# Kernel tuning notes

Measured on AMD Instinct MI355X. Metric: run time of the kernel, lower is better.

## Reference

```python
import jax, jax.numpy as jnp
import numpy as np

N_NODES = 50000
N_EDGES = 800000
IN_FEATS = 1024
LAYERS = [128, 128]
EPS = 1e-5  # BatchNorm1d eps


def setup_inputs() -> dict:
    key = jax.random.key(0)
    ks = jax.random.split(key, 24)
    inp = {}
    inp["in_feat"] = jax.random.normal(ks[0], (N_NODES, IN_FEATS), jnp.float32)
    inp["src"] = jax.random.randint(ks[1], (N_EDGES,), 0, N_NODES, dtype=jnp.int32)
    inp["dst"] = jax.random.randint(ks[2], (N_EDGES,), 0, N_NODES, dtype=jnp.int32)
    dims = [IN_FEATS] + LAYERS
    i = 3
    for l in range(len(LAYERS)):
        din, dout = dims[l], dims[l + 1]
        s = 1.0 / np.sqrt(din)
        inp[f"W{l}"] = jax.random.uniform(ks[i], (din, dout), jnp.float32, -s, s); i += 1
        inp[f"b{l}"] = jnp.zeros((dout,), jnp.float32)
        inp[f"Wr{l}"] = jax.random.uniform(ks[i], (din, dout), jnp.float32, -s, s); i += 1
        inp[f"br{l}"] = jnp.zeros((dout,), jnp.float32)
        inp[f"gamma{l}"] = jnp.ones((dout,), jnp.float32)
        inp[f"beta{l}"] = jnp.zeros((dout,), jnp.float32)
        inp[f"mean{l}"] = jnp.zeros((dout,), jnp.float32)
        inp[f"var{l}"] = jnp.ones((dout,), jnp.float32)
    s = 1.0 / np.sqrt(LAYERS[-1])
    inp["Wd"] = jax.random.uniform(ks[i], (LAYERS[-1], 2), jnp.float32, -s, s)
    inp["bd"] = jnp.zeros((2,), jnp.float32)
    return inp


def gcn_layer(h, src, dst, W, b, Wr, br, gamma, beta, mean, var):
    # dgllife GCNLayer: GraphConv(norm='none', activation=relu) -> residual -> dropout(id, eval) -> BN(eval)
    msg = (h @ W)[src]                                        # [E, dout] gather of transformed src feats
    agg = jax.ops.segment_sum(msg, dst, num_segments=N_NODES)  # scatter-add to dst nodes
    new = jax.nn.relu(agg + b)                                 # GraphConv bias + activation
    res = jax.nn.relu(h @ Wr + br)                             # residual Linear + activation
    new = new + res
    return (new - mean) * jax.lax.rsqrt(var + EPS) * gamma + beta  # BatchNorm1d eval


def reference(in_feat, src, dst,
              W0, b0, Wr0, br0, gamma0, beta0, mean0, var0,
              W1, b1, Wr1, br1, gamma1, beta1, mean1, var1,
              Wd, bd):
    h = gcn_layer(in_feat, src, dst, W0, b0, Wr0, br0, gamma0, beta0, mean0, var0)
    h = gcn_layer(h, src, dst, W1, b1, Wr1, br1, gamma1, beta1, mean1, var1)
    logits = h @ Wd + bd                                       # [N, 2]
    return jax.nn.softmax(logits, axis=1)
```

## Files before the change

kernel.cpp:

```cpp
#include <hip/hip_runtime.h>
#include <math.h>

#define NNODES 50000
#define NEDGES 800000
#define KIN 1024
#define DH 128

typedef __bf16 bf16x8 __attribute__((ext_vector_type(8)));
typedef float floatx4 __attribute__((ext_vector_type(4)));

__global__ void k_zero2(int* __restrict__ a, int* __restrict__ b, int n) {
  int i = blockIdx.x * blockDim.x + threadIdx.x;
  if (i < n) { a[i] = 0; b[i] = 0; }
}

__global__ void k_hist(const int* __restrict__ dst, int* __restrict__ cnt, int E) {
  int i = blockIdx.x * blockDim.x + threadIdx.x;
  if (i < E) atomicAdd(&cnt[dst[i]], 1);
}

__global__ __launch_bounds__(1024) void k_scan_local(const int* __restrict__ cnt,
                                                     int* __restrict__ row_ptr,
                                                     int* __restrict__ bsum, int n) {
  __shared__ int sd[1024];
  int t = threadIdx.x;
  int i = blockIdx.x * 1024 + t;
  int v = (i < n) ? cnt[i] : 0;
  sd[t] = v;
  __syncthreads();
  for (int off = 1; off < 1024; off <<= 1) {
    int tv = (t >= off) ? sd[t - off] : 0;
    __syncthreads();
    sd[t] += tv;
    __syncthreads();
  }
  if (i < n) row_ptr[i] = sd[t] - v;
  if (t == 1023) bsum[blockIdx.x] = sd[t];
}

__global__ void k_scan_sums(const int* __restrict__ bsum, int* __restrict__ boff,
                            int nb, int* __restrict__ row_ptr, int n) {
  int lane = threadIdx.x;
  int v = (lane < nb) ? bsum[lane] : 0;
  int incl = v;
  for (int off = 1; off < 64; off <<= 1) {
    int t = __shfl_up(incl, off);
    if (lane >= off) incl += t;
  }
  boff[lane] = incl - v;
  if (lane == 63) row_ptr[n] = incl;
}

__global__ void k_scan_add(int* __restrict__ row_ptr, const int* __restrict__ boff, int n) {
  int i = blockIdx.x * blockDim.x + threadIdx.x;
  if (i < n) row_ptr[i] += boff[i >> 10];
}

__global__ void k_fill(const int* __restrict__ src, const int* __restrict__ dst,
                       const int* __restrict__ row_ptr, int* __restrict__ cursor,
                       int* __restrict__ csr_src, int E) {
  int i = blockIdx.x * blockDim.x + threadIdx.x;
  if (i < E) {
    int d = dst[i];
    int pos = row_ptr[d] + atomicAdd(&cursor[d], 1);
    csr_src[pos] = src[i];
  }
}

__global__ __launch_bounds__(256) void k_prepB(const float* __restrict__ W,
                                               const float* __restrict__ Wr,
                                               __bf16* __restrict__ Bt, int K, int kbits) {
  int id = blockIdx.x * 256 + threadIdx.x;
  int k = id & (K - 1);
  int n = id >> kbits;
  float v = (n < DH) ? W[(size_t)k * DH + n] : Wr[(size_t)k * DH + (n - DH)];
  Bt[(size_t)n * K + k] = (__bf16)v;
}

__device__ __forceinline__ void load_lds16(const void* g, void* l) {
  __builtin_amdgcn_global_load_lds(
      (const __attribute__((address_space(1))) unsigned int*)g,
      (__attribute__((address_space(3))) unsigned int*)l, 16, 0, 0);
}

#define WAITV(N) asm volatile("s_waitcnt vmcnt(" #N ")" ::: "memory")

template <typename AT, int K>
__global__ __launch_bounds__(512, 2) void k_gemm_mfma(
    const AT* __restrict__ X, const __bf16* __restrict__ Bt,
    const float* __restrict__ br, __bf16* __restrict__ XW,
    float* __restrict__ RES, int M) {
  constexpr int ROWB = (sizeof(AT) == 4) ? 256 : 128;
  constexpr int ABUF = 64 * ROWB;
  constexpr int BBUF = 256 * 64 * 2;
  constexpr int TBUF = ABUF + BBUF;
  __shared__ alignas(16) char smem[3 * TBUF];
  const int tid = threadIdx.x;
  const int lane = tid & 63;
  const int w = tid >> 6;
  const int wr = w >> 2;
  const int wc = w & 3;
  const int l15 = lane & 15;
  const int quad = lane >> 4;
  const int bm0 = blockIdx.x * 64;

  auto stageA = [&](char* abase, int k0) {
    if constexpr (sizeof(AT) == 4) {
#pragma unroll
      for (int i = 0; i < 2; ++i) {
        const int r = w * 8 + i * 4 + (lane >> 4);
        int gr = bm0 + r; if (gr > M - 1) gr = M - 1;
        const int c = (lane & 15) ^ (r & 7);
        load_lds16((const char*)X + ((size_t)gr * K + k0 + c * 4) * 4,
                   abase + (w * 8 + i * 4) * 256);
      }
    } else {
      const int r = w * 8 + (lane >> 3);
      int gr = bm0 + r; if (gr > M - 1) gr = M - 1;
      const int c = (lane & 7) ^ (r & 7);
      load_lds16((const char*)X + ((size_t)gr * K + k0 + c * 8) * 2,
                 abase + w * 8 * 128);
    }
  };
  auto stageB = [&](char* bbase, int k0) {
#pragma unroll
    for (int ii = 0; ii < 4; ++ii) {
      const int wi = ii * 8 + w;
      const int n = wi * 8 + (lane >> 3);
      const int c = lane & 7;
      const int cs = c ^ (n & 7);
      load_lds16((const char*)Bt + (size_t)n * (K * 2) + (size_t)k0 * 2 + cs * 16,
                 bbase + wi * 1024);
    }
  };
  auto stage = [&](int s) {
    char* base = smem + (s % 3) * TBUF;
    stageA(base, s * 64);
    stageB(base + ABUF, s * 64);
  };

  auto readA = [&](const char* abase, int mt, int ks) -> bf16x8 {
    const int r = wr * 32 + mt * 16 + l15;
    const char* rowp = abase + r * ROWB;
    if constexpr (sizeof(AT) == 4) {
      const int x = r & 7;
      const int c0 = ks * 8 + quad * 2;
      const floatx4 u = *(const floatx4*)(rowp + ((c0 ^ x) << 4));
      const floatx4 v = *(const floatx4*)(rowp + (((c0 + 1) ^ x) << 4));
      bf16x8 h;
      h[0] = (__bf16)u[0]; h[1] = (__bf16)u[1]; h[2] = (__bf16)u[2]; h[3] = (__bf16)u[3];
      h[4] = (__bf16)v[0]; h[5] = (__bf16)v[1]; h[6] = (__bf16)v[2]; h[7] = (__bf16)v[3];
      return h;
    } else {
      const int cc = ks * 4 + quad;
      return *(const bf16x8*)(rowp + ((cc ^ (r & 7)) << 4));
    }
  };
  auto readB = [&](const char* bbase, int nt, int ks) -> bf16x8 {
    const int n = wc * 64 + nt * 16 + l15;
    const int ch = (ks * 4 + quad) ^ (n & 7);
    return *(const bf16x8*)(bbase + n * 128 + ch * 16);
  };

  floatx4 acc[2][4];
#pragma unroll
  for (int i = 0; i < 2; ++i)
#pragma unroll
    for (int j = 0; j < 4; ++j) acc[i][j] = (floatx4)0.f;

  constexpr int NS = K / 64;
  stage(0);
  stage(1);

  for (int s = 0; s < NS; ++s) {
    if (s == NS - 1) {
      WAITV(0);
    } else if constexpr (sizeof(AT) == 4) {
      WAITV(6);
    } else {
      WAITV(5);
    }
    __builtin_amdgcn_s_barrier();
    __builtin_amdgcn_sched_barrier(0);
    if (s + 2 < NS) stage(s + 2);
    const char* abase = smem + (s % 3) * TBUF;
    const char* bbase = abase + ABUF;
    bf16x8 af[2][2], bfr[4][2];
#pragma unroll
    for (int mt = 0; mt < 2; ++mt)
#pragma unroll
      for (int ks = 0; ks < 2; ++ks) af[mt][ks] = readA(abase, mt, ks);
#pragma unroll
    for (int nt = 0; nt < 4; ++nt)
#pragma unroll
      for (int ks = 0; ks < 2; ++ks) bfr[nt][ks] = readB(bbase, nt, ks);
#pragma unroll
    for (int ks = 0; ks < 2; ++ks)
#pragma unroll
      for (int mt = 0; mt < 2; ++mt)
#pragma unroll
        for (int nt = 0; nt < 4; ++nt)
          acc[mt][nt] = __builtin_amdgcn_mfma_f32_16x16x32_bf16(af[mt][ks], bfr[nt][ks],
                                                                acc[mt][nt], 0, 0, 0);
  }
  __syncthreads();

  float* Cb = (float*)smem;
#pragma unroll
  for (int half = 0; half < 2; ++half) {
    if (wr == half) {
#pragma unroll
      for (int mt = 0; mt < 2; ++mt)
#pragma unroll
        for (int nt = 0; nt < 4; ++nt)
#pragma unroll
          for (int r = 0; r < 4; ++r)
            Cb[(mt * 16 + quad * 4 + r) * 256 + wc * 64 + nt * 16 + l15] = acc[mt][nt][r];
    }
    __syncthreads();
    const int row = tid >> 4;
    const int seg = tid & 15;
    const int grow = bm0 + half * 32 + row;
    if (grow < M) {
      if (seg < 8) {
        const int c0 = seg * 16;
#pragma unroll
        for (int j = 0; j < 2; ++j) {
          const float4 v0 = *(const float4*)&Cb[row * 256 + c0 + j * 8];
          const float4 v1 = *(const float4*)&Cb[row * 256 + c0 + j * 8 + 4];
          bf16x8 h;
          h[0] = (__bf16)v0.x; h[1] = (__bf16)v0.y; h[2] = (__bf16)v0.z; h[3] = (__bf16)v0.w;
          h[4] = (__bf16)v1.x; h[5] = (__bf16)v1.y; h[6] = (__bf16)v1.z; h[7] = (__bf16)v1.w;
          *(bf16x8*)&XW[(size_t)grow * DH + c0 + j * 8] = h;
        }
      } else {
        const int c0 = (seg - 8) * 16;
#pragma unroll
        for (int j = 0; j < 4; ++j) {
          const float4 v = *(const float4*)&Cb[row * 256 + 128 + c0 + j * 4];
          const float4 bb = *(const float4*)&br[c0 + j * 4];
          *(float4*)&RES[(size_t)grow * DH + c0 + j * 4] =
              make_float4(fmaxf(v.x + bb.x, 0.f), fmaxf(v.y + bb.y, 0.f),
                          fmaxf(v.z + bb.z, 0.f), fmaxf(v.w + bb.w, 0.f));
        }
      }
    }
    __syncthreads();
  }
}

template <int MODE>
__global__ __launch_bounds__(256) void k_agg2(
    const __bf16* __restrict__ XW, const float* __restrict__ RES,
    const int* __restrict__ row_ptr, const int* __restrict__ csr_src,
    const float* __restrict__ b, const float* __restrict__ gamma,
    const float* __restrict__ beta, const float* __restrict__ mean,
    const float* __restrict__ var, const float* __restrict__ Wd,
    const float* __restrict__ bd, void* __restrict__ hout, int M) {
  const int node = (blockIdx.x << 2) + (threadIdx.x >> 6);
  const int lane = threadIdx.x & 63;
  if (node >= M) return;
  const int s = row_ptr[node], e = row_ptr[node + 1];
  const unsigned* xw = (const unsigned*)XW;
  float ax = 0.f, ay = 0.f;
  int i = s;
  for (; i + 3 < e; i += 4) {
    const int s0 = csr_src[i], s1 = csr_src[i + 1], s2 = csr_src[i + 2], s3 = csr_src[i + 3];
    const unsigned u0 = xw[(size_t)s0 * 64 + lane];
    const unsigned u1 = xw[(size_t)s1 * 64 + lane];
    const unsigned u2 = xw[(size_t)s2 * 64 + lane];
    const unsigned u3 = xw[(size_t)s3 * 64 + lane];
    ax += __uint_as_float(u0 << 16) + __uint_as_float(u1 << 16) +
          __uint_as_float(u2 << 16) + __uint_as_float(u3 << 16);
    ay += __uint_as_float(u0 & 0xffff0000u) + __uint_as_float(u1 & 0xffff0000u) +
          __uint_as_float(u2 & 0xffff0000u) + __uint_as_float(u3 & 0xffff0000u);
  }
  for (; i < e; ++i) {
    const unsigned u = xw[(size_t)csr_src[i] * 64 + lane];
    ax += __uint_as_float(u << 16);
    ay += __uint_as_float(u & 0xffff0000u);
  }
  const int f0 = lane << 1;
  const float2 bb = *(const float2*)&b[f0];
  const float2 rr = *(const float2*)&RES[(size_t)node * DH + f0];
  const float2 mm = *(const float2*)&mean[f0];
  const float2 vv = *(const float2*)&var[f0];
  const float2 gg = *(const float2*)&gamma[f0];
  const float2 be = *(const float2*)&beta[f0];
  const float x0 = fmaxf(ax + bb.x, 0.f) + rr.x;
  const float x1 = fmaxf(ay + bb.y, 0.f) + rr.y;
  const float y0 = (x0 - mm.x) * rsqrtf(vv.x + 1e-5f) * gg.x + be.x;
  const float y1 = (x1 - mm.y) * rsqrtf(vv.y + 1e-5f) * gg.y + be.y;
  if (MODE == 0) {
    union { __bf16 h[2]; unsigned u; } pk;
    pk.h[0] = (__bf16)y0;
    pk.h[1] = (__bf16)y1;
    ((unsigned*)hout)[(size_t)node * 64 + lane] = pk.u;
  } else {
    const float4 wv = *(const float4*)&Wd[f0 * 2];
    float l0 = y0 * wv.x + y1 * wv.z;
    float l1 = y0 * wv.y + y1 * wv.w;
#pragma unroll
    for (int off = 32; off > 0; off >>= 1) {
      l0 += __shfl_down(l0, off);
      l1 += __shfl_down(l1, off);
    }
    if (lane == 0) {
      l0 += bd[0];
      l1 += bd[1];
      const float m = fmaxf(l0, l1);
      const float e0 = expf(l0 - m), e1 = expf(l1 - m);
      const float inv = 1.f / (e0 + e1);
      float* out = (float*)hout;
      out[(size_t)node * 2] = e0 * inv;
      out[(size_t)node * 2 + 1] = e1 * inv;
    }
  }
}

extern "C" void kernel_launch(void* const* d_in, const int* in_sizes, int n_in,
                              void* d_out, int out_size, void* d_ws, size_t ws_size,
                              hipStream_t stream) {
  const float* in_feat = (const float*)d_in[0];
  const int* src = (const int*)d_in[1];
  const int* dst = (const int*)d_in[2];
  const float* W0 = (const float*)d_in[3];
  const float* b0 = (const float*)d_in[4];
  const float* Wr0 = (const float*)d_in[5];
  const float* br0 = (const float*)d_in[6];
  const float* gamma0 = (const float*)d_in[7];
  const float* beta0 = (const float*)d_in[8];
  const float* mean0 = (const float*)d_in[9];
  const float* var0 = (const float*)d_in[10];
  const float* W1 = (const float*)d_in[11];
  const float* b1 = (const float*)d_in[12];
  const float* Wr1 = (const float*)d_in[13];
  const float* br1 = (const float*)d_in[14];
  const float* gamma1 = (const float*)d_in[15];
  const float* beta1 = (const float*)d_in[16];
  const float* mean1 = (const float*)d_in[17];
  const float* var1 = (const float*)d_in[18];
  const float* Wd = (const float*)d_in[19];
  const float* bd = (const float*)d_in[20];
  float* out = (float*)d_out;

  char* ws = (char*)d_ws;
  size_t off = 0;
  auto alloc = [&](size_t bytes) {
    void* p = ws + off;
    off += (bytes + 255) & ~(size_t)255;
    return p;
  };
  __bf16* XWb = (__bf16*)alloc(sizeof(__bf16) * (size_t)NNODES * DH);
  __bf16* h1 = (__bf16*)alloc(sizeof(__bf16) * (size_t)NNODES * DH);
  float* RES = (float*)alloc(sizeof(float) * (size_t)NNODES * DH);
  int* cnt = (int*)alloc(sizeof(int) * NNODES);
  int* cursor = (int*)alloc(sizeof(int) * NNODES);
  int* row_ptr = (int*)alloc(sizeof(int) * (NNODES + 1));
  int* csr_src = (int*)alloc(sizeof(int) * NEDGES);
  int* bsum = (int*)alloc(sizeof(int) * 64);
  int* boff = (int*)alloc(sizeof(int) * 64);
  __bf16* Bt0 = (__bf16*)alloc(sizeof(__bf16) * 256 * KIN);
  __bf16* Bt1 = (__bf16*)alloc(sizeof(__bf16) * 256 * DH);

  const int nb = (NNODES + 1023) / 1024;
  k_zero2<<<(NNODES + 255) / 256, 256, 0, stream>>>(cnt, cursor, NNODES);
  k_hist<<<(NEDGES + 255) / 256, 256, 0, stream>>>(dst, cnt, NEDGES);
  k_scan_local<<<nb, 1024, 0, stream>>>(cnt, row_ptr, bsum, NNODES);
  k_scan_sums<<<1, 64, 0, stream>>>(bsum, boff, nb, row_ptr, NNODES);
  k_scan_add<<<(NNODES + 255) / 256, 256, 0, stream>>>(row_ptr, boff, NNODES);
  k_fill<<<(NEDGES + 255) / 256, 256, 0, stream>>>(src, dst, row_ptr, cursor, csr_src, NEDGES);

  k_prepB<<<KIN, 256, 0, stream>>>(W0, Wr0, Bt0, KIN, 10);
  k_prepB<<<DH, 256, 0, stream>>>(W1, Wr1, Bt1, DH, 7);

  const int ggrid = (NNODES + 63) / 64;
  const int agrid = (NNODES + 3) / 4;
  k_gemm_mfma<float, KIN><<<ggrid, 512, 0, stream>>>(in_feat, Bt0, br0, XWb, RES, NNODES);
  k_agg2<0><<<agrid, 256, 0, stream>>>(XWb, RES, row_ptr, csr_src, b0, gamma0, beta0,
                                       mean0, var0, nullptr, nullptr, h1, NNODES);
  k_gemm_mfma<__bf16, DH><<<ggrid, 512, 0, stream>>>(h1, Bt1, br1, XWb, RES, NNODES);
  k_agg2<1><<<agrid, 256, 0, stream>>>(XWb, RES, row_ptr, csr_src, b1, gamma1, beta1,
                                       mean1, var1, Wd, bd, out, NNODES);
}
```

Before: 551.5 us.

## Halve fp32 GEMM K-tile to cut LDS and raise occupancy; add nontemporal A loads

For the fp32-input GEMM (the first layer, K=1024), the K step drops from 64 to 32, shrinking the LDS per stage so four 512-thread blocks can fit per CU instead of two (launch bounds raised). The A-operand loads into LDS now use a nontemporal cache hint, since X is streamed once. MFMA sections are wrapped in s_setprio to favour issuing the compute. The cost is twice as many pipeline stages and barriers for the fp32 path, and the higher occupancy target may force register pressure or spills.

```diff
diff --git a/kernel.cpp b/kernel.cpp
--- a/kernel.cpp
+++ b/kernel.cpp
@@ -82,17 +82,24 @@
       (const __attribute__((address_space(1))) unsigned int*)g,
       (__attribute__((address_space(3))) unsigned int*)l, 16, 0, 0);
 }
+__device__ __forceinline__ void load_lds16_nt(const void* g, void* l) {
+  __builtin_amdgcn_global_load_lds(
+      (const __attribute__((address_space(1))) unsigned int*)g,
+      (__attribute__((address_space(3))) unsigned int*)l, 16, 0, 2 );
+}
 
 #define WAITV(N) asm volatile("s_waitcnt vmcnt(" #N ")" ::: "memory")
 
 template <typename AT, int K>
-__global__ __launch_bounds__(512, 2) void k_gemm_mfma(
+__global__ __launch_bounds__(512, 4) void k_gemm_mfma(
     const AT* __restrict__ X, const __bf16* __restrict__ Bt,
     const float* __restrict__ br, __bf16* __restrict__ XW,
     float* __restrict__ RES, int M) {
-  constexpr int ROWB = (sizeof(AT) == 4) ? 256 : 128;
+  constexpr int BK = (sizeof(AT) == 4) ? 32 : 64;
+  constexpr int ROWB = 128;
   constexpr int ABUF = 64 * ROWB;
-  constexpr int BBUF = 256 * 64 * 2;
+  constexpr int BROWB = BK * 2;
+  constexpr int BBUF = 256 * BROWB;
   constexpr int TBUF = ABUF + BBUF;
   __shared__ alignas(16) char smem[3 * TBUF];
   const int tid = threadIdx.x;
@@ -104,47 +111,48 @@
   const int quad = lane >> 4;
   const int bm0 = blockIdx.x * 64;
 
-  auto stageA = [&](char* abase, int k0) {
-    if constexpr (sizeof(AT) == 4) {
-#pragma unroll
-      for (int i = 0; i < 2; ++i) {
-        const int r = w * 8 + i * 4 + (lane >> 4);
-        int gr = bm0 + r; if (gr > M - 1) gr = M - 1;
-        const int c = (lane & 15) ^ (r & 7);
-        load_lds16((const char*)X + ((size_t)gr * K + k0 + c * 4) * 4,
-                   abase + (w * 8 + i * 4) * 256);
+  auto stage = [&](int s2) {
+    char* base = smem + (s2 % 3) * TBUF;
+    {
+      const int r = w * 8 + (lane >> 3);
+      int gr = bm0 + r; if (gr > M - 1) gr = M - 1;
+      const int cs = (lane & 7) ^ (r & 7);
+      if constexpr (sizeof(AT) == 4) {
+        load_lds16_nt((const char*)X + ((size_t)gr * K + s2 * BK + cs * 4) * 4,
+                      base + w * 1024);
+      } else {
+        load_lds16_nt((const char*)X + ((size_t)gr * K + s2 * BK + cs * 8) * 2,
+                      base + w * 1024);
+      }
+    }
+    char* bbase = base + ABUF;
+    if constexpr (BK == 32) {
+#pragma unroll
+      for (int ii = 0; ii < 2; ++ii) {
+        const int wi = ii * 8 + w;
+        const int n = wi * 16 + (lane >> 2);
+        const int cs = (lane & 3) ^ (n & 3);
+        load_lds16((const char*)Bt + (size_t)n * (K * 2) + (size_t)(s2 * BK) * 2 + cs * 16,
+                   bbase + wi * 1024);
       }
     } else {
-      const int r = w * 8 + (lane >> 3);
-      int gr = bm0 + r; if (gr > M - 1) gr = M - 1;
-      const int c = (lane & 7) ^ (r & 7);
-      load_lds16((const char*)X + ((size_t)gr * K + k0 + c * 8) * 2,
-                 abase + w * 8 * 128);
-    }
-  };
-  auto stageB = [&](char* bbase, int k0) {
-#pragma unroll
-    for (int ii = 0; ii < 4; ++ii) {
-      const int wi = ii * 8 + w;
-      const int n = wi * 8 + (lane >> 3);
-      const int c = lane & 7;
-      const int cs = c ^ (n & 7);
-      load_lds16((const char*)Bt + (size_t)n * (K * 2) + (size_t)k0 * 2 + cs * 16,
-                 bbase + wi * 1024);
-    }
-  };
-  auto stage = [&](int s) {
-    char* base = smem + (s % 3) * TBUF;
-    stageA(base, s * 64);
-    stageB(base + ABUF, s * 64);
+#pragma unroll
+      for (int ii = 0; ii < 4; ++ii) {
+        const int wi = ii * 8 + w;
+        const int n = wi * 8 + (lane >> 3);
+        const int cs = (lane & 7) ^ (n & 7);
+        load_lds16((const char*)Bt + (size_t)n * (K * 2) + (size_t)(s2 * BK) * 2 + cs * 16,
+                   bbase + wi * 1024);
+      }
+    }
   };
 
   auto readA = [&](const char* abase, int mt, int ks) -> bf16x8 {
     const int r = wr * 32 + mt * 16 + l15;
     const char* rowp = abase + r * ROWB;
+    const int x = r & 7;
     if constexpr (sizeof(AT) == 4) {
-      const int x = r & 7;
-      const int c0 = ks * 8 + quad * 2;
+      const int c0 = quad * 2;
       const floatx4 u = *(const floatx4*)(rowp + ((c0 ^ x) << 4));
       const floatx4 v = *(const floatx4*)(rowp + (((c0 + 1) ^ x) << 4));
       bf16x8 h;
@@ -153,13 +161,18 @@
       return h;
     } else {
       const int cc = ks * 4 + quad;
-      return *(const bf16x8*)(rowp + ((cc ^ (r & 7)) << 4));
+      return *(const bf16x8*)(rowp + ((cc ^ x) << 4));
     }
   };
   auto readB = [&](const char* bbase, int nt, int ks) -> bf16x8 {
     const int n = wc * 64 + nt * 16 + l15;
-    const int ch = (ks * 4 + quad) ^ (n & 7);
-    return *(const bf16x8*)(bbase + n * 128 + ch * 16);
+    if constexpr (BK == 32) {
+      const int ch = quad ^ (n & 3);
+      return *(const bf16x8*)(bbase + n * 64 + ch * 16);
+    } else {
+      const int ch = (ks * 4 + quad) ^ (n & 7);
+      return *(const bf16x8*)(bbase + n * 128 + ch * 16);
+    }
   };
 
   floatx4 acc[2][4];
@@ -168,15 +181,15 @@
 #pragma unroll
     for (int j = 0; j < 4; ++j) acc[i][j] = (floatx4)0.f;
 
-  constexpr int NS = K / 64;
+  constexpr int NS = K / BK;
   stage(0);
   stage(1);
 
   for (int s = 0; s < NS; ++s) {
     if (s == NS - 1) {
       WAITV(0);
-    } else if constexpr (sizeof(AT) == 4) {
-      WAITV(6);
+    } else if constexpr (BK == 32) {
+      WAITV(3);
     } else {
       WAITV(5);
     }
@@ -185,23 +198,41 @@
     if (s + 2 < NS) stage(s + 2);
     const char* abase = smem + (s % 3) * TBUF;
     const char* bbase = abase + ABUF;
-    bf16x8 af[2][2], bfr[4][2];
-#pragma unroll
-    for (int mt = 0; mt < 2; ++mt)
-#pragma unroll
-      for (int ks = 0; ks < 2; ++ks) af[mt][ks] = readA(abase, mt, ks);
-#pragma unroll
-    for (int nt = 0; nt < 4; ++nt)
-#pragma unroll
-      for (int ks = 0; ks < 2; ++ks) bfr[nt][ks] = readB(bbase, nt, ks);
-#pragma unroll
-    for (int ks = 0; ks < 2; ++ks)
+    if constexpr (BK == 32) {
+      bf16x8 af[2], bfr[4];
+#pragma unroll
+      for (int mt = 0; mt < 2; ++mt) af[mt] = readA(abase, mt, 0);
+#pragma unroll
+      for (int nt = 0; nt < 4; ++nt) bfr[nt] = readB(bbase, nt, 0);
+      __builtin_amdgcn_s_setprio(1);
 #pragma unroll
       for (int mt = 0; mt < 2; ++mt)
 #pragma unroll
         for (int nt = 0; nt < 4; ++nt)
-          acc[mt][nt] = __builtin_amdgcn_mfma_f32_16x16x32_bf16(af[mt][ks], bfr[nt][ks],
+          acc[mt][nt] = __builtin_amdgcn_mfma_f32_16x16x32_bf16(af[mt], bfr[nt],
                                                                 acc[mt][nt], 0, 0, 0);
+      __builtin_amdgcn_s_setprio(0);
+    } else {
+      bf16x8 af[2][2], bfr[4][2];
+#pragma unroll
+      for (int mt = 0; mt < 2; ++mt)
+#pragma unroll
+        for (int ks = 0; ks < 2; ++ks) af[mt][ks] = readA(abase, mt, ks);
+#pragma unroll
+      for (int nt = 0; nt < 4; ++nt)
+#pragma unroll
+        for (int ks = 0; ks < 2; ++ks) bfr[nt][ks] = readB(bbase, nt, ks);
+      __builtin_amdgcn_s_setprio(1);
+#pragma unroll
+      for (int ks = 0; ks < 2; ++ks)
+#pragma unroll
+        for (int mt = 0; mt < 2; ++mt)
+#pragma unroll
+          for (int nt = 0; nt < 4; ++nt)
+            acc[mt][nt] = __builtin_amdgcn_mfma_f32_16x16x32_bf16(af[mt][ks], bfr[nt][ks],
+                                                                  acc[mt][nt], 0, 0, 0);
+      __builtin_amdgcn_s_setprio(0);
+    }
   }
   __syncthreads();
 
```

Measured after the change: 556.1 us. About the same (+0.8%).
